# Kernel tuning notes

Hardware: AMD Instinct MI355X
Metric: run time of the kernel (lower is better)

The kernel has to match this reference:

```python
import jax, jax.numpy as jnp
import numpy as np
from math import factorial

ZETA = [1, 2, 3, 4]          # configs['zeta']=4 -> range(1,5)
NZETA = len(ZETA)
NRAD = 16
NLAMBDA = 2
NAT = 4000
NEDGE = 100000
ZMAX = max(ZETA)


def _make_lxlylz(zmax):
    tr, fn = [], []
    for s in range(zmax + 1):
        for lx in range(s + 1):
            for ly in range(s - lx + 1):
                lz = s - lx - ly
                tr.append((lx, ly, lz))
                fn.append(factorial(s) / (factorial(lx) * factorial(ly) * factorial(lz)))
    return np.asarray(tr, np.int32), np.asarray(fn, np.float32)


def setup_inputs() -> dict:
    key = jax.random.key(0)
    k1, k2, k3, k4 = jax.random.split(key, 4)
    rij = jax.random.normal(k1, (NEDGE, 3), dtype=jnp.float32)
    rij_unit = rij / jnp.linalg.norm(rij, axis=-1, keepdims=True)
    radial_ij = jax.random.uniform(k2, (NEDGE, NRAD, NZETA + 1), dtype=jnp.float32)
    lambda_weights = jax.random.normal(k3, (NLAMBDA,), dtype=jnp.float32)
    first_atom_idx = jnp.sort(jax.random.randint(k4, (NEDGE,), 0, NAT, dtype=jnp.int32))
    tr, fn = _make_lxlylz(ZMAX)
    return {
        "rij_unit": rij_unit,
        "radial_ij": radial_ij,
        "lambda_weights": lambda_weights,
        "fact_norm": jnp.asarray(fn),
        "first_atom_idx": first_atom_idx,
        "lxlylz": jnp.asarray(tr),
        "lxlylz_sum": jnp.asarray(tr.sum(axis=-1).astype(np.int32)),
        "nat": NAT,
    }


def reference(rij_unit, radial_ij, lambda_weights, fact_norm,
              first_atom_idx, lxlylz, lxlylz_sum, nat):
    # angular monomials g_ij_lxlylz : [E, L]
    lf = lxlylz.astype(jnp.float32)
    g_ij = jnp.prod(rij_unit[:, None, :] ** lf[None, :, :], axis=-1) * fact_norm[None, :]
    # lambda^(lx+ly+lz) : [n_lambda, L]
    lam = lambda_weights[:, None] ** lxlylz_sum.astype(jnp.float32)[None, :]
    # two-body radial descriptor: segment-sum of last radial channel -> [nat, Nrad]
    radial_i = jax.ops.segment_sum(radial_ij[:, :, -1], first_atom_idx, num_segments=nat)
    feats = [radial_i]
    for r_idx, z in enumerate(ZETA):
        # gather-compute: [E, Nrad, L]
        g = jnp.einsum('ej,ek->ejk', radial_ij[:, :, r_idx], g_ij)
        # scatter-reduce over neighbors of each central atom -> [nat, Nrad, L]
        g_i = jax.ops.segment_sum(g, first_atom_idx, num_segments=nat)
        # three-body power contraction with lambda weights, norm 2^(1-z)
        gi3 = jnp.einsum('njk,lk->njl', g_i * g_i, lam) * jnp.float32(2.0 ** (1.0 - z))
        feats.append(gi3.reshape(nat, -1))
    return jnp.concatenate(feats, axis=-1)  # [nat, Nrad*(1 + n_lambda*nzeta)]
```

## Files before the change

### kernel.cpp

```cpp
#include <hip/hip_runtime.h>

#define NRAD 16
#define NCH  5
#define NMON 35
#define OUTW 144
#define TILE 64
#define ROWF (NRAD * NCH)

__global__ __launch_bounds__(256) void seg_offsets(
    const int* __restrict__ idx, int* __restrict__ seg, int E, int nat)
{
    int e = blockIdx.x * blockDim.x + threadIdx.x;
    if (e >= E) return;
    if (e == 0) {
        const int b = idx[0];
        for (int n = 0; n <= b; ++n) seg[n] = 0;
    } else {
        const int a = idx[e - 1], b = idx[e];
        for (int n = a + 1; n <= b; ++n) seg[n] = e;
    }
    if (e == E - 1) {
        const int a = idx[E - 1];
        for (int n = a + 1; n <= nat; ++n) seg[n] = E;
    }
}

__device__ __forceinline__ void edge_body(
    float x, float y, float z, float rad, float c4,
    float acc[NMON], float& acc2)
{
    const float x2 = x * x, x3 = x2 * x, x4 = x2 * x2;
    const float y2 = y * y, y3 = y2 * y, y4 = y2 * y2;
    const float z2 = z * z, z3 = z2 * z, z4 = z2 * z2;
    const float xy = x * y, xz = x * z, yz = y * z;

    acc2 += c4;
    acc[0]  += rad;
    acc[1]  = fmaf(rad, z,        acc[1]);
    acc[2]  = fmaf(rad, y,        acc[2]);
    acc[3]  = fmaf(rad, x,        acc[3]);
    acc[4]  = fmaf(rad, z2,       acc[4]);
    acc[5]  = fmaf(rad, yz,       acc[5]);
    acc[6]  = fmaf(rad, y2,       acc[6]);
    acc[7]  = fmaf(rad, xz,       acc[7]);
    acc[8]  = fmaf(rad, xy,       acc[8]);
    acc[9]  = fmaf(rad, x2,       acc[9]);
    acc[10] = fmaf(rad, z3,       acc[10]);
    acc[11] = fmaf(rad, y * z2,   acc[11]);
    acc[12] = fmaf(rad, y2 * z,   acc[12]);
    acc[13] = fmaf(rad, y3,       acc[13]);
    acc[14] = fmaf(rad, x * z2,   acc[14]);
    acc[15] = fmaf(rad, xy * z,   acc[15]);
    acc[16] = fmaf(rad, x * y2,   acc[16]);
    acc[17] = fmaf(rad, x2 * z,   acc[17]);
    acc[18] = fmaf(rad, x2 * y,   acc[18]);
    acc[19] = fmaf(rad, x3,       acc[19]);
    acc[20] = fmaf(rad, z4,       acc[20]);
    acc[21] = fmaf(rad, y * z3,   acc[21]);
    acc[22] = fmaf(rad, y2 * z2,  acc[22]);
    acc[23] = fmaf(rad, y3 * z,   acc[23]);
    acc[24] = fmaf(rad, y4,       acc[24]);
    acc[25] = fmaf(rad, x * z3,   acc[25]);
    acc[26] = fmaf(rad, xy * z2,  acc[26]);
    acc[27] = fmaf(rad, x * y2 * z, acc[27]);
    acc[28] = fmaf(rad, x * y3,   acc[28]);
    acc[29] = fmaf(rad, x2 * z2,  acc[29]);
    acc[30] = fmaf(rad, x2 * yz,  acc[30]);
    acc[31] = fmaf(rad, x2 * y2,  acc[31]);
    acc[32] = fmaf(rad, x3 * z,   acc[32]);
    acc[33] = fmaf(rad, x3 * y,   acc[33]);
    acc[34] = fmaf(rad, x4,       acc[34]);
}

__global__ __launch_bounds__(256) void mbp_main(
    const float* __restrict__ rij_unit,
    const float* __restrict__ radial_ij,
    const float* __restrict__ lambda_w,
    const float* __restrict__ fact_norm,
    const int*   __restrict__ seg,
    float* __restrict__ out,
    int nat)
{
    __shared__ float rad_t[TILE * ROWF];
    __shared__ float rij_t[TILE * 3];

    const int n    = blockIdx.x;
    const int tid  = threadIdx.x;
    const int wave = tid >> 6;
    const int lane = tid & 63;
    const int zi   = lane >> 4;
    const int r    = lane & 15;

    const int start = seg[n];
    const int end   = seg[n + 1];

    float acc[NMON];
    #pragma unroll
    for (int l = 0; l < NMON; ++l) acc[l] = 0.f;
    float acc2 = 0.f;

    for (int ts = start; ts < end; ts += TILE) {
        const int T = min(TILE, end - ts);

        {
            const float4* __restrict__ src = (const float4*)(radial_ij + (size_t)ts * ROWF);
            float4* dst = (float4*)rad_t;
            const int nf4 = T * (ROWF / 4);
            for (int i = tid; i < nf4; i += 256) dst[i] = src[i];
        }
        for (int i = tid; i < T * 3; i += 256) rij_t[i] = rij_unit[(size_t)ts * 3 + i];
        __syncthreads();

        for (int j = wave; j < T; j += 4) {
            const float x   = rij_t[j * 3 + 0];
            const float y   = rij_t[j * 3 + 1];
            const float z   = rij_t[j * 3 + 2];
            const float rad = rad_t[j * ROWF + r * NCH + zi];
            const float c4  = rad_t[j * ROWF + r * NCH + 4];
            edge_body(x, y, z, rad, c4, acc, acc2);
        }
        __syncthreads();
    }

    float* red = rad_t;
    const int region = wave >> 1;
    const int rbase  = region * (NMON + 1) * 64;

    if (wave & 1) {
        #pragma unroll
        for (int l = 0; l < NMON; ++l) red[rbase + l * 64 + lane] = acc[l];
        red[rbase + NMON * 64 + lane] = acc2;
    }
    __syncthreads();
    if (!(wave & 1)) {
        #pragma unroll
        for (int l = 0; l < NMON; ++l) acc[l] += red[rbase + l * 64 + lane];
        acc2 += red[rbase + NMON * 64 + lane];
    }
    __syncthreads();
    if (wave == 2) {
        #pragma unroll
        for (int l = 0; l < NMON; ++l) red[rbase + l * 64 + lane] = acc[l];
        red[rbase + NMON * 64 + lane] = acc2;
    }
    __syncthreads();
    if (wave != 0) return;

    const int r1base = (NMON + 1) * 64;
    #pragma unroll
    for (int l = 0; l < NMON; ++l) acc[l] += red[r1base + l * 64 + lane];
    acc2 += red[r1base + NMON * 64 + lane];

    const float l0 = lambda_w[0], l1 = lambda_w[1];
    const float p0[5] = {1.f, l0, l0 * l0, l0 * l0 * l0, (l0 * l0) * (l0 * l0)};
    const float p1[5] = {1.f, l1, l1 * l1, l1 * l1 * l1, (l1 * l1) * (l1 * l1)};
    const int lsum_tab[NMON] = {0, 1,1,1, 2,2,2,2,2,2,
                                3,3,3,3,3,3,3,3,3,3,
                                4,4,4,4,4,4,4,4,4,4,4,4,4,4,4};
    float s0 = 0.f, s1 = 0.f;
    #pragma unroll
    for (int l = 0; l < NMON; ++l) {
        const float v = acc[l] * fact_norm[l];
        const float v2 = v * v;
        s0 = fmaf(v2, p0[lsum_tab[l]], s0);
        s1 = fmaf(v2, p1[lsum_tab[l]], s1);
    }
    const float scale = 1.0f / (float)(1 << zi);
    float* orow = out + (long)n * OUTW;
    orow[16 + zi * 32 + r * 2 + 0] = s0 * scale;
    orow[16 + zi * 32 + r * 2 + 1] = s1 * scale;
    if (zi == 0) orow[r] = acc2;
}

extern "C" void kernel_launch(void* const* d_in, const int* in_sizes, int n_in,
                              void* d_out, int out_size, void* d_ws, size_t ws_size,
                              hipStream_t stream) {
    const float* rij_unit   = (const float*)d_in[0];
    const float* radial_ij  = (const float*)d_in[1];
    const float* lambda_w   = (const float*)d_in[2];
    const float* fact_norm  = (const float*)d_in[3];
    const int*   first_atom = (const int*)d_in[4];
    const int E   = in_sizes[4];
    const int nat = out_size / OUTW;

    int* seg = (int*)d_ws;

    seg_offsets<<<(E + 255) / 256, 256, 0, stream>>>(first_atom, seg, E, nat);
    mbp_main<<<nat, 256, 0, stream>>>(rij_unit, radial_ij, lambda_w,
                                      fact_norm, seg, (float*)d_out, nat);
}
```

Measured before the change: 107.8 us.

## Process each atom with a single wave reading edges directly from global memory

Replaces the 256-thread block per atom, which staged edge tiles in LDS, with a 64-thread single-wave kernel that loads radial and unit-vector data straight from global memory per edge. This removes the shared-memory staging, the barriers and the multi-wave LDS reduction. In exchange, each wave loops serially over all edges of its atom, so latency hiding has to come from more resident blocks rather than from parallelism within a block.

After: 107.3 us. Within noise of the previous version (-0.5%).

```diff
diff --git a/kernel.cpp b/kernel.cpp
--- a/kernel.cpp
+++ b/kernel.cpp
@@ -4,7 +4,6 @@
 #define NCH  5
 #define NMON 35
 #define OUTW 144
-#define TILE 64
 #define ROWF (NRAD * NCH)
 
 __global__ __launch_bounds__(256) void seg_offsets(
@@ -72,22 +71,16 @@
     acc[34] = fmaf(rad, x4,       acc[34]);
 }
 
-__global__ __launch_bounds__(256) void mbp_main(
+__global__ __launch_bounds__(64) void mbp_wave(
     const float* __restrict__ rij_unit,
     const float* __restrict__ radial_ij,
     const float* __restrict__ lambda_w,
     const float* __restrict__ fact_norm,
     const int*   __restrict__ seg,
-    float* __restrict__ out,
-    int nat)
+    float* __restrict__ out)
 {
-    __shared__ float rad_t[TILE * ROWF];
-    __shared__ float rij_t[TILE * 3];
-
     const int n    = blockIdx.x;
-    const int tid  = threadIdx.x;
-    const int wave = tid >> 6;
-    const int lane = tid & 63;
+    const int lane = threadIdx.x;
     const int zi   = lane >> 4;
     const int r    = lane & 15;
 
@@ -99,57 +92,19 @@
     for (int l = 0; l < NMON; ++l) acc[l] = 0.f;
     float acc2 = 0.f;
 
-    for (int ts = start; ts < end; ts += TILE) {
-        const int T = min(TILE, end - ts);
+    const int off  = r * NCH + zi;
+    const int off4 = r * NCH + 4;
 
-        {
-            const float4* __restrict__ src = (const float4*)(radial_ij + (size_t)ts * ROWF);
-            float4* dst = (float4*)rad_t;
-            const int nf4 = T * (ROWF / 4);
-            for (int i = tid; i < nf4; i += 256) dst[i] = src[i];
-        }
-        for (int i = tid; i < T * 3; i += 256) rij_t[i] = rij_unit[(size_t)ts * 3 + i];
-        __syncthreads();
-
-        for (int j = wave; j < T; j += 4) {
-            const float x   = rij_t[j * 3 + 0];
-            const float y   = rij_t[j * 3 + 1];
-            const float z   = rij_t[j * 3 + 2];
-            const float rad = rad_t[j * ROWF + r * NCH + zi];
-            const float c4  = rad_t[j * ROWF + r * NCH + 4];
-            edge_body(x, y, z, rad, c4, acc, acc2);
-        }
-        __syncthreads();
+    #pragma unroll 2
+    for (int e = start; e < end; ++e) {
+        const float* __restrict__ row = radial_ij + (size_t)e * ROWF;
+        const float rad = row[off];
+        const float c4  = row[off4];
+        const float x   = rij_unit[3 * e + 0];
+        const float y   = rij_unit[3 * e + 1];
+        const float z   = rij_unit[3 * e + 2];
+        edge_body(x, y, z, rad, c4, acc, acc2);
     }
-
-    float* red = rad_t;
-    const int region = wave >> 1;
-    const int rbase  = region * (NMON + 1) * 64;
-
-    if (wave & 1) {
-        #pragma unroll
-        for (int l = 0; l < NMON; ++l) red[rbase + l * 64 + lane] = acc[l];
-        red[rbase + NMON * 64 + lane] = acc2;
-    }
-    __syncthreads();
-    if (!(wave & 1)) {
-        #pragma unroll
-        for (int l = 0; l < NMON; ++l) acc[l] += red[rbase + l * 64 + lane];
-        acc2 += red[rbase + NMON * 64 + lane];
-    }
-    __syncthreads();
-    if (wave == 2) {
-        #pragma unroll
-        for (int l = 0; l < NMON; ++l) red[rbase + l * 64 + lane] = acc[l];
-        red[rbase + NMON * 64 + lane] = acc2;
-    }
-    __syncthreads();
-    if (wave != 0) return;
-
-    const int r1base = (NMON + 1) * 64;
-    #pragma unroll
-    for (int l = 0; l < NMON; ++l) acc[l] += red[r1base + l * 64 + lane];
-    acc2 += red[r1base + NMON * 64 + lane];
 
     const float l0 = lambda_w[0], l1 = lambda_w[1];
     const float p0[5] = {1.f, l0, l0 * l0, l0 * l0 * l0, (l0 * l0) * (l0 * l0)};
@@ -160,7 +115,7 @@
     float s0 = 0.f, s1 = 0.f;
     #pragma unroll
     for (int l = 0; l < NMON; ++l) {
-        const float v = acc[l] * fact_norm[l];
+        const float v  = acc[l] * fact_norm[l];
         const float v2 = v * v;
         s0 = fmaf(v2, p0[lsum_tab[l]], s0);
         s1 = fmaf(v2, p1[lsum_tab[l]], s1);
@@ -186,6 +141,6 @@
     int* seg = (int*)d_ws;
 
     seg_offsets<<<(E + 255) / 256, 256, 0, stream>>>(first_atom, seg, E, nat);
-    mbp_main<<<nat, 256, 0, stream>>>(rij_unit, radial_ij, lambda_w,
-                                      fact_norm, seg, (float*)d_out, nat);
+    mbp_wave<<<nat, 64, 0, stream>>>(rij_unit, radial_ij, lambda_w,
+                                     fact_norm, seg, (float*)d_out);
 }
```
